# Kernel optimization log

Hardware: AMD Instinct MI355X
Metric: run time of the kernel (lower is better)

## Reference

```python
import jax, jax.numpy as jnp
import numpy as np

B, N, E, H, D, FF, L = 64, 200, 128, 8, 16, 512, 6
S = N + 1  # depot + nodes
EPS = 1e-5


def setup_inputs() -> dict:
    key = jax.random.key(0)
    ks = jax.random.split(key, 24)
    r = jax.random.normal
    HD = H * D
    inp = {
        "depot_xy": jax.random.uniform(ks[0], (B, 1, 3), dtype=jnp.float32),
        "node_xy_demand_tw": jax.random.uniform(ks[1], (B, N, 4), dtype=jnp.float32),
        "route_attn": r(ks[2], (B, H, S, S), dtype=jnp.float32),
        # initial embeddings
        "Wd": r(ks[3], (3, E)) * 0.3, "bd": jnp.zeros((E,)),
        "Wn": r(ks[4], (4, E)) * 0.3, "bn": jnp.zeros((E,)),
        # per-layer stacked params (leading dim L)
        "Wq": r(ks[5], (L, E, HD)) / np.sqrt(E),
        "Wk": r(ks[6], (L, E, HD)) / np.sqrt(E),
        "Wv": r(ks[7], (L, E, HD)) / np.sqrt(E),
        "Wo": r(ks[8], (L, HD, E)) / np.sqrt(HD), "bo": jnp.zeros((L, E)),
        # score_aggr MLP: in=head_num*aspect_num=2H, hidden=2H, out=H
        "A1w": r(ks[9], (L, 2 * H, 2 * H)) / np.sqrt(2 * H), "A1b": jnp.zeros((L, 2 * H)),
        "A2w": r(ks[10], (L, 2 * H, H)) / np.sqrt(2 * H), "A2b": jnp.zeros((L, H)),
        # instance-norm affine params
        "n1w": jnp.ones((L, E)), "n1b": jnp.zeros((L, E)),
        "n2w": jnp.ones((L, E)), "n2b": jnp.zeros((L, E)),
        # feed-forward
        "F1w": r(ks[11], (L, E, FF)) / np.sqrt(E), "F1b": jnp.zeros((L, FF)),
        "F2w": r(ks[12], (L, FF, E)) / np.sqrt(FF), "F2b": jnp.zeros((L, E)),
    }
    return inp


def _inorm(y, w, b):
    # InstanceNorm1d over the sequence axis (per batch, per channel), biased var, eps=1e-5
    m = jnp.mean(y, axis=1, keepdims=True)
    v = jnp.var(y, axis=1, keepdims=True)
    return (y - m) / jnp.sqrt(v + EPS) * w + b


def _encoder(depot_xy, node_xy_demand_tw, route_attn, Wd, bd, Wn, bn,
             Wq, Wk, Wv, Wo, bo, A1w, A1b, A2w, A2b,
             n1w, n1b, n2w, n2b, F1w, F1b, F2w, F2b):
    x = jnp.concatenate([depot_xy @ Wd + bd, node_xy_demand_tw @ Wn + bn], axis=1)  # [B,S,E]
    b, s = x.shape[0], x.shape[1]
    for l in range(L):
        heads = lambda t: t.reshape(b, s, H, D).transpose(0, 2, 1, 3)  # [B,H,S,D]
        q, k, v = heads(x @ Wq[l]), heads(x @ Wk[l]), heads(x @ Wv[l])
        score = jnp.einsum('bhnd,bhmd->bhnm', q, k)                    # [B,H,S,S]
        cat = jnp.concatenate([score, route_attn], axis=1)             # [B,2H,S,S]
        cat = cat.transpose(0, 2, 3, 1)                                # [B,S,S,2H]
        agg = jax.nn.relu(cat @ A1w[l] + A1b[l]) @ A2w[l] + A2b[l]     # [B,S,S,H]
        scaled = agg.transpose(0, 3, 1, 2)                             # [B,H,S,S]
        w = jax.nn.softmax(scaled, axis=-1)
        o = jnp.einsum('bhnm,bhmd->bhnd', w, v)                        # [B,H,S,D]
        o = o.transpose(0, 2, 1, 3).reshape(b, s, H * D)
        mh = o @ Wo[l] + bo[l]
        out1 = _inorm(x + mh, n1w[l], n1b[l])
        ff = jax.nn.relu(out1 @ F1w[l] + F1b[l]) @ F2w[l] + F2b[l]
        x = _inorm(out1 + ff, n2w[l], n2b[l])
    return x


def reference(depot_xy, node_xy_demand_tw, route_attn, Wd, bd, Wn, bn,
              Wq, Wk, Wv, Wo, bo, A1w, A1b, A2w, A2b,
              n1w, n1b, n2w, n2b, F1w, F1b, F2w, F2b):
    return _encoder(depot_xy, node_xy_demand_tw, route_attn, Wd, bd, Wn, bn,
                    Wq, Wk, Wv, Wo, bo, A1w, A1b, A2w, A2b,
                    n1w, n1b, n2w, n2b, F1w, F1b, F2w, F2b)
```

## Files before the change

kernel.cpp:

```cpp
#include <hip/hip_runtime.h>
#include <hip/hip_bf16.h>

#define B_   64
#define N_   200
#define S_   201
#define E_   128
#define H_   8
#define D_   16
#define HD_  128
#define FF_  512
#define L_   6
#define TWOH_ 16
#define NCH_  4
#define NCHB_ 51
#define PADM_ 209
#define QKVW_ 384

typedef __hip_bfloat16 bf16;
typedef __attribute__((ext_vector_type(8))) short bfrag;
typedef __attribute__((ext_vector_type(4))) float f32x4;

__device__ __forceinline__ void split_bf16(float v, bf16& h, bf16& l) {
  h = __float2bfloat16(v);
  l = __float2bfloat16(v - __bfloat162float(h));
}

__device__ __forceinline__ void stage16(const bf16* g, bf16* l) {
  __builtin_amdgcn_global_load_lds(
      (const __attribute__((address_space(1))) void*)g,
      (__attribute__((address_space(3))) void*)l, 16, 0, 0);
}

__global__ void embed_kernel(const float* __restrict__ depot, const float* __restrict__ node,
                             const float* __restrict__ Wd, const float* __restrict__ bd,
                             const float* __restrict__ Wn, const float* __restrict__ bn,
                             float* __restrict__ X, bf16* __restrict__ XBh, bf16* __restrict__ XBl) {
  int idx = blockIdx.x * blockDim.x + threadIdx.x;
  if (idx >= B_ * S_ * E_) return;
  int e  = idx & (E_ - 1);
  int bs = idx >> 7;
  int s  = bs % S_;
  int b  = bs / S_;
  float acc;
  if (s == 0) {
    acc = bd[e];
    #pragma unroll
    for (int i = 0; i < 3; ++i) acc += depot[b * 3 + i] * Wd[i * E_ + e];
  } else {
    acc = bn[e];
    const float* nd = node + ((size_t)b * N_ + (s - 1)) * 4;
    #pragma unroll
    for (int i = 0; i < 4; ++i) acc += nd[i] * Wn[i * E_ + e];
  }
  X[idx] = acc;
  bf16 hh, ll;
  split_bf16(acc, hh, ll);
  XBh[idx] = hh;
  XBl[idx] = ll;
}

__global__ void wcvt_kernel(const float* __restrict__ Wo, const float* __restrict__ F1w,
                            const float* __restrict__ F2w, const float* __restrict__ Wq,
                            const float* __restrict__ Wk, const float* __restrict__ Wv,
                            bf16* __restrict__ WTh, bf16* __restrict__ WTl) {
  int idx = blockIdx.x * blockDim.x + threadIdx.x;
  if (idx >= 1179648) return;
  float v;
  if (idx < 98304) {
    int l = idx / 16384, rr = idx % 16384;
    int e = rr / 128, h = rr % 128;
    v = Wo[(size_t)l * 16384 + h * 128 + e];
  } else if (idx < 491520) {
    int rem = idx - 98304;
    int l = rem / 65536, rr = rem % 65536;
    int f = rr / 128, e = rr % 128;
    v = F1w[(size_t)l * 65536 + e * 512 + f];
  } else if (idx < 884736) {
    int rem = idx - 491520;
    int l = rem / 65536, rr = rem % 65536;
    int e = rr / 512, f = rr % 512;
    v = F2w[(size_t)l * 65536 + f * 128 + e];
  } else {
    int rem = idx - 884736;
    int l = rem / 49152, rr = rem % 49152;
    int n = rr / 128, e = rr % 128;
    const float* src = (n < 128) ? Wq : (n < 256) ? Wk : Wv;
    int hd = n & 127;
    v = src[(size_t)l * 16384 + e * 128 + hd];
  }
  bf16 h, l2;
  split_bf16(v, h, l2);
  WTh[idx] = h;
  WTl[idx] = l2;
}

template<int EPI>
__global__ __launch_bounds__(256) void mgemm_kernel(
    const bf16* __restrict__ Ah, const bf16* __restrict__ Al,
    const bf16* __restrict__ BTh, const bf16* __restrict__ BTl,
    const float* __restrict__ bias, const float* __restrict__ res,
    float* __restrict__ Cf, bf16* __restrict__ Cbh, bf16* __restrict__ Cbl,
    int K, int Ntot, int lda) {
  __shared__ __align__(16) bf16 Ash[4096];
  __shared__ __align__(16) bf16 Asl[4096];
  __shared__ __align__(16) bf16 Bsh[4096];
  __shared__ __align__(16) bf16 Bsl[4096];
  int tid = threadIdx.x;
  int m0 = blockIdx.x * 64, n0 = blockIdx.y * 64;
  int lane = tid & 63, wave = tid >> 6;
  int wr = wave >> 1, wc = wave & 1;
  int la = lane & 15, lb = lane >> 4;
  int lrow = lane >> 3;
  int cbl  = (lane & 7) ^ (lrow & 7);
  f32x4 acc[2][2] = {};
  for (int k0 = 0; k0 < K; k0 += 64) {
    #pragma unroll
    for (int c = 0; c < 2; ++c) {
      int rr = wave * 16 + c * 8 + lrow;
      size_t ga = (size_t)(m0 + rr) * lda + k0 + cbl * 8;
      size_t gb = (size_t)(n0 + rr) * K + k0 + cbl * 8;
      int lo = wave * 1024 + c * 512;
      stage16(Ah + ga, Ash + lo);
      stage16(Al + ga, Asl + lo);
      stage16(BTh + gb, Bsh + lo);
      stage16(BTl + gb, Bsl + lo);
    }
    __syncthreads();
    #pragma unroll
    for (int ks = 0; ks < 64; ks += 32) {
      int cb0 = (ks >> 3) + lb;
      auto rd = [&](const bf16* buf, int r) {
        return *reinterpret_cast<const bfrag*>(&buf[r * 64 + ((cb0 ^ (r & 7)) << 3)]);
      };
      int ra0 = wr * 32 + la, ra1 = ra0 + 16;
      int rb0 = wc * 32 + la, rb1 = rb0 + 16;
      bfrag ah0 = rd(Ash, ra0), ah1 = rd(Ash, ra1);
      bfrag al0 = rd(Asl, ra0), al1 = rd(Asl, ra1);
      bfrag bh0 = rd(Bsh, rb0), bh1 = rd(Bsh, rb1);
      bfrag bl0 = rd(Bsl, rb0), bl1 = rd(Bsl, rb1);
      acc[0][0] = __builtin_amdgcn_mfma_f32_16x16x32_bf16(ah0, bh0, acc[0][0], 0, 0, 0);
      acc[0][0] = __builtin_amdgcn_mfma_f32_16x16x32_bf16(ah0, bl0, acc[0][0], 0, 0, 0);
      acc[0][0] = __builtin_amdgcn_mfma_f32_16x16x32_bf16(al0, bh0, acc[0][0], 0, 0, 0);
      acc[0][1] = __builtin_amdgcn_mfma_f32_16x16x32_bf16(ah0, bh1, acc[0][1], 0, 0, 0);
      acc[0][1] = __builtin_amdgcn_mfma_f32_16x16x32_bf16(ah0, bl1, acc[0][1], 0, 0, 0);
      acc[0][1] = __builtin_amdgcn_mfma_f32_16x16x32_bf16(al0, bh1, acc[0][1], 0, 0, 0);
      acc[1][0] = __builtin_amdgcn_mfma_f32_16x16x32_bf16(ah1, bh0, acc[1][0], 0, 0, 0);
      acc[1][0] = __builtin_amdgcn_mfma_f32_16x16x32_bf16(ah1, bl0, acc[1][0], 0, 0, 0);
      acc[1][0] = __builtin_amdgcn_mfma_f32_16x16x32_bf16(al1, bh0, acc[1][0], 0, 0, 0);
      acc[1][1] = __builtin_amdgcn_mfma_f32_16x16x32_bf16(ah1, bh1, acc[1][1], 0, 0, 0);
      acc[1][1] = __builtin_amdgcn_mfma_f32_16x16x32_bf16(ah1, bl1, acc[1][1], 0, 0, 0);
      acc[1][1] = __builtin_amdgcn_mfma_f32_16x16x32_bf16(al1, bh1, acc[1][1], 0, 0, 0);
    }
    __syncthreads();
  }
  int r0 = lb * 4;
  #pragma unroll
  for (int ti = 0; ti < 2; ++ti)
    #pragma unroll
    for (int tj = 0; tj < 2; ++tj)
      #pragma unroll
      for (int j = 0; j < 4; ++j) {
        int m = m0 + wr * 32 + ti * 16 + r0 + j;
        int n = n0 + wc * 32 + tj * 16 + la;
        float v = acc[ti][tj][j];
        if (EPI == 1) {
          v += bias[n] + res[(size_t)m * Ntot + n];
          Cf[(size_t)m * Ntot + n] = v;
        } else if (EPI == 2) {
          v += bias[n];
          v = v > 0.f ? v : 0.f;
          bf16 vh, vl;
          split_bf16(v, vh, vl);
          Cbh[(size_t)m * Ntot + n] = vh;
          Cbl[(size_t)m * Ntot + n] = vl;
        } else {
          Cf[(size_t)m * Ntot + n] = v;
        }
      }
}

__global__ __launch_bounds__(256) void score_kernel(const float* __restrict__ QKV,
                                                    float* __restrict__ SC) {
  int bh = blockIdx.x;
  int h = bh & 7, b = bh >> 3;
  int nbase = blockIdx.y * 51;
  int ncnt = min(51, S_ - nbase);
  __shared__ __align__(16) float qs[51][20];
  __shared__ __align__(16) float ks[S_][20];
  int tid = threadIdx.x;
  for (int p = tid; p < 51 * 16; p += 256) {
    int r = p >> 4, d = p & 15;
    if (r < ncnt) qs[r][d] = QKV[((size_t)(b * S_ + nbase + r)) * QKVW_ + h * D_ + d];
  }
  for (int p = tid; p < S_ * 16; p += 256) {
    int r = p >> 4, d = p & 15;
    ks[r][d] = QKV[((size_t)(b * S_ + r)) * QKVW_ + 128 + h * D_ + d];
  }
  __syncthreads();
  float* out = SC + ((size_t)(b * H_ + h)) * S_ * S_;
  int tn = tid >> 4, tm = tid & 15;
  for (int n0 = tn * 2; n0 < ncnt; n0 += 32) {
    int n1v = (n0 + 1 < ncnt);
    f32x4 q0[4], q1[4];
    #pragma unroll
    for (int qd = 0; qd < 4; ++qd) {
      q0[qd] = *(const f32x4*)&qs[n0][qd * 4];
      q1[qd] = *(const f32x4*)&qs[n1v ? n0 + 1 : n0][qd * 4];
    }
    for (int m0 = tm * 2; m0 < S_; m0 += 32) {
      int m1v = (m0 + 1 < S_);
      float a00 = 0, a01 = 0, a10 = 0, a11 = 0;
      #pragma unroll
      for (int qd = 0; qd < 4; ++qd) {
        f32x4 k0 = *(const f32x4*)&ks[m0][qd * 4];
        f32x4 k1 = *(const f32x4*)&ks[m1v ? m0 + 1 : m0][qd * 4];
        #pragma unroll
        for (int c = 0; c < 4; ++c) {
          a00 += q0[qd][c] * k0[c];
          a01 += q0[qd][c] * k1[c];
          a10 += q1[qd][c] * k0[c];
          a11 += q1[qd][c] * k1[c];
        }
      }
      int gn = nbase + n0;
      out[(size_t)gn * S_ + m0] = a00;
      if (m1v) out[(size_t)gn * S_ + m0 + 1] = a01;
      if (n1v) {
        out[(size_t)(gn + 1) * S_ + m0] = a10;
        if (m1v) out[(size_t)(gn + 1) * S_ + m0 + 1] = a11;
      }
    }
  }
}

__global__ __launch_bounds__(256) void attn_kernel(
    const float* __restrict__ SC, const float* __restrict__ RA,
    const float* __restrict__ A1w, const float* __restrict__ A1b,
    const float* __restrict__ A2w, const float* __restrict__ A2b,
    float* __restrict__ QKV) {
  int blk = blockIdx.x;
  int b  = blk / NCHB_;
  int n0 = (blk % NCHB_) * NCH_;
  int NV = min(NCH_, S_ - n0);
  __shared__ float PL[NCH_][H_][PADM_];
  __shared__ float partial[2][NCH_][H_][D_];
  __shared__ float inv[NCH_][H_];
  int tid = threadIdx.x;

  {
    float cc[4][TWOH_];
    int   mm[4], nnv[4];
    bool  val[4];
    #pragma unroll
    for (int s = 0; s < 4; ++s) {
      int e = tid + s * 256;
      val[s] = (e < NV * S_);
      int nn = e / S_;
      int m  = e - nn * S_;
      if (!val[s]) { nn = 0; m = 0; }
      nnv[s] = nn; mm[s] = m;
      const float* scp = SC + (((size_t)b * H_) * S_ + (n0 + nn)) * S_ + m;
      const float* rap = RA + (((size_t)b * H_) * S_ + (n0 + nn)) * S_ + m;
      #pragma unroll
      for (int h = 0; h < H_; ++h) {
        cc[s][h]      = scp[(size_t)h * S_ * S_];
        cc[s][H_ + h] = rap[(size_t)h * S_ * S_];
      }
    }
    #pragma unroll
    for (int s = 0; s < 4; ++s) {
      if (!val[s]) continue;
      float h1[TWOH_];
      #pragma unroll
      for (int j = 0; j < TWOH_; ++j) h1[j] = A1b[j];
      #pragma unroll
      for (int i = 0; i < TWOH_; ++i) {
        float c = cc[s][i];
        #pragma unroll
        for (int j = 0; j < TWOH_; ++j)
          h1[j] += c * A1w[i * TWOH_ + j];
      }
      float agg[H_];
      #pragma unroll
      for (int h = 0; h < H_; ++h) agg[h] = A2b[h];
      #pragma unroll
      for (int j = 0; j < TWOH_; ++j) {
        float r = fmaxf(h1[j], 0.f);
        #pragma unroll
        for (int h = 0; h < H_; ++h)
          agg[h] += r * A2w[j * H_ + h];
      }
      #pragma unroll
      for (int h = 0; h < H_; ++h) PL[nnv[s]][h][mm[s]] = agg[h];
    }
  }
  __syncthreads();

  {
    int g = tid >> 3, lane = tid & 7;
    int nn = g >> 3, h = g & 7;
    if (nn < NV) {
      float mx = -1e30f;
      for (int m = lane; m < S_; m += 8) mx = fmaxf(mx, PL[nn][h][m]);
      #pragma unroll
      for (int off = 4; off > 0; off >>= 1) mx = fmaxf(mx, __shfl_xor(mx, off, 8));
      float sum = 0.f;
      for (int m = lane; m < S_; m += 8) {
        float e = __expf(PL[nn][h][m] - mx);
        PL[nn][h][m] = e;
        sum += e;
      }
      #pragma unroll
      for (int off = 4; off > 0; off >>= 1) sum += __shfl_xor(sum, off, 8);
      if (lane == 0) inv[nn][h] = 1.f / sum;
    }
  }
  __syncthreads();

  {
    int half = tid >> 7, h = (tid >> 4) & 7, d = tid & 15;
    float a0 = 0.f, a1 = 0.f, a2 = 0.f, a3 = 0.f;
    const float* vp = QKV + (size_t)b * S_ * QKVW_ + 256 + h * D_ + d;
    for (int m = half; m < S_; m += 2) {
      float vv = vp[(size_t)m * QKVW_];
      a0 += PL[0][h][m] * vv;
      a1 += PL[1][h][m] * vv;
      a2 += PL[2][h][m] * vv;
      a3 += PL[3][h][m] * vv;
    }
    partial[half][0][h][d] = a0;
    partial[half][1][h][d] = a1;
    partial[half][2][h][d] = a2;
    partial[half][3][h][d] = a3;
  }
  __syncthreads();
  if (tid < 128) {
    int h = tid >> 4, d = tid & 15;
    #pragma unroll
    for (int nn = 0; nn < NCH_; ++nn)
      if (nn < NV) {
        float s = (partial[0][nn][h][d] + partial[1][nn][h][d]) * inv[nn][h];
        bf16* ob = (bf16*)(QKV + (size_t)(b * S_ + n0 + nn) * QKVW_);
        bf16 sh, sl;
        split_bf16(s, sh, sl);
        ob[h * D_ + d]       = sh;
        ob[128 + h * D_ + d] = sl;
      }
  }
}

__global__ __launch_bounds__(128) void inorm_kernel(const float* __restrict__ Y,
                                                    const float* __restrict__ w,
                                                    const float* __restrict__ bb,
                                                    float* __restrict__ X,
                                                    bf16* __restrict__ XBh,
                                                    bf16* __restrict__ XBl) {
  int b = blockIdx.x;
  int e0 = blockIdx.y * 32;
  int tid = threadIdx.x;
  int el = tid & 31, sg = tid >> 5;
  int e = e0 + el;
  __shared__ float ps[4][32], pss[4][32];
  const float* base = Y + (size_t)b * S_ * E_;
  float s = 0.f, ss = 0.f;
  for (int i = sg; i < S_; i += 4) {
    float v = base[(size_t)i * E_ + e];
    s += v; ss += v * v;
  }
  ps[sg][el] = s; pss[sg][el] = ss;
  __syncthreads();
  if (sg == 0) {
    s  = ps[0][el] + ps[1][el] + ps[2][el] + ps[3][el];
    ss = pss[0][el] + pss[1][el] + pss[2][el] + pss[3][el];
    float mean = s / S_;
    float var  = fmaxf(ss / S_ - mean * mean, 0.f);
    float scale = rsqrtf(var + 1e-5f) * w[e];
    ps[0][el]  = scale;
    pss[0][el] = bb[e] - mean * scale;
  }
  __syncthreads();
  float scale = ps[0][el], shift = pss[0][el];
  float* dst = X + (size_t)b * S_ * E_;
  for (int i = sg; i < S_; i += 4) {
    size_t idx = (size_t)i * E_ + e;
    float v = base[idx] * scale + shift;
    dst[idx] = v;
    if (XBh) {
      size_t gi = (size_t)b * S_ * E_ + idx;
      bf16 vh, vl;
      split_bf16(v, vh, vl);
      XBh[gi] = vh;
      XBl[gi] = vl;
    }
  }
}

extern "C" void kernel_launch(void* const* d_in, const int* in_sizes, int n_in,
                              void* d_out, int out_size, void* d_ws, size_t ws_size,
                              hipStream_t stream) {
  const float* depot = (const float*)d_in[0];
  const float* node  = (const float*)d_in[1];
  const float* RA    = (const float*)d_in[2];
  const float* Wd    = (const float*)d_in[3];
  const float* bd    = (const float*)d_in[4];
  const float* Wn    = (const float*)d_in[5];
  const float* bn    = (const float*)d_in[6];
  const float* Wq    = (const float*)d_in[7];
  const float* Wk    = (const float*)d_in[8];
  const float* Wv    = (const float*)d_in[9];
  const float* Wo    = (const float*)d_in[10];
  const float* bo    = (const float*)d_in[11];
  const float* A1w   = (const float*)d_in[12];
  const float* A1b   = (const float*)d_in[13];
  const float* A2w   = (const float*)d_in[14];
  const float* A2b   = (const float*)d_in[15];
  const float* n1w   = (const float*)d_in[16];
  const float* n1b   = (const float*)d_in[17];
  const float* n2w   = (const float*)d_in[18];
  const float* n2b   = (const float*)d_in[19];
  const float* F1w   = (const float*)d_in[20];
  const float* F1b   = (const float*)d_in[21];
  const float* F2w   = (const float*)d_in[22];
  const float* F2b   = (const float*)d_in[23];

  const size_t XSZ  = (size_t)B_ * S_ * E_;
  const size_t SCSZ = (size_t)B_ * H_ * S_ * S_;
  const size_t XBF  = XSZ / 2;
  float* ws = (float*)d_ws;
  float* X   = ws;
  float* QKV = ws + XSZ;
  float* SC  = ws + 4 * XSZ;
  float* TMP = SC;
  bf16*  XBh = (bf16*)(SC + XSZ);
  bf16*  XBl = (bf16*)(SC + XSZ + XBF);
  bf16*  HBh = (bf16*)(SC + XSZ + 2 * XBF);
  bf16*  HBl = (bf16*)(SC + XSZ + 6 * XBF);
  float* tail = ws + 4 * XSZ + SCSZ;
  bf16*  WTh = (bf16*)tail;
  bf16*  WTl = (bf16*)(tail + 589824);
  const bf16* OBh = (const bf16*)QKV;
  const bf16* OBl = (const bf16*)QKV + 128;

  const int M = B_ * S_;

  wcvt_kernel<<<4608, 256, 0, stream>>>(Wo, F1w, F2w, Wq, Wk, Wv, WTh, WTl);
  embed_kernel<<<(B_ * S_ * E_ + 255) / 256, 256, 0, stream>>>(depot, node, Wd, bd, Wn, bn, X, XBh, XBl);

  for (int l = 0; l < L_; ++l) {
    mgemm_kernel<3><<<dim3(M / 64, 6), 256, 0, stream>>>(
        XBh, XBl, WTh + 884736 + (size_t)l * 49152, WTl + 884736 + (size_t)l * 49152,
        nullptr, nullptr, QKV, nullptr, nullptr, E_, QKVW_, E_);
    score_kernel<<<dim3(B_ * H_, 4), 256, 0, stream>>>(QKV, SC);
    attn_kernel<<<B_ * NCHB_, 256, 0, stream>>>(SC, RA,
        A1w + (size_t)l * TWOH_ * TWOH_, A1b + (size_t)l * TWOH_,
        A2w + (size_t)l * TWOH_ * H_,    A2b + (size_t)l * H_, QKV);
    mgemm_kernel<1><<<dim3(M / 64, 2), 256, 0, stream>>>(
        OBh, OBl, WTh + (size_t)l * 16384, WTl + (size_t)l * 16384,
        bo + (size_t)l * E_, X, TMP, nullptr, nullptr, HD_, E_, 768);
    inorm_kernel<<<dim3(B_, 4), 128, 0, stream>>>(TMP, n1w + (size_t)l * E_, n1b + (size_t)l * E_, X, XBh, XBl);
    mgemm_kernel<2><<<dim3(M / 64, 8), 256, 0, stream>>>(
        XBh, XBl, WTh + 98304 + (size_t)l * 65536, WTl + 98304 + (size_t)l * 65536,
        F1b + (size_t)l * FF_, nullptr, nullptr, HBh, HBl, E_, FF_, E_);
    mgemm_kernel<1><<<dim3(M / 64, 2), 256, 0, stream>>>(
        HBh, HBl, WTh + 491520 + (size_t)l * 65536, WTl + 491520 + (size_t)l * 65536,
        F2b + (size_t)l * E_, X, TMP, nullptr, nullptr, FF_, E_, FF_);
    float* dst = (l == L_ - 1) ? (float*)d_out : X;
    bf16* xh = (l == L_ - 1) ? nullptr : XBh;
    bf16* xl = (l == L_ - 1) ? nullptr : XBl;
    inorm_kernel<<<dim3(B_, 4), 128, 0, stream>>>(TMP, n2w + (size_t)l * E_, n2b + (size_t)l * E_, dst, xh, xl);
  }
}
```

Measured before the change: 1.476 ms.

## Fuse QK score computation into attention kernel, dropping score buffer

Result: faster. 1.358 ms (-8.0%).

```diff
diff --git a/kernel.cpp b/kernel.cpp
--- a/kernel.cpp
+++ b/kernel.cpp
@@ -179,62 +179,8 @@
       }
 }
 
-__global__ __launch_bounds__(256) void score_kernel(const float* __restrict__ QKV,
-                                                    float* __restrict__ SC) {
-  int bh = blockIdx.x;
-  int h = bh & 7, b = bh >> 3;
-  int nbase = blockIdx.y * 51;
-  int ncnt = min(51, S_ - nbase);
-  __shared__ __align__(16) float qs[51][20];
-  __shared__ __align__(16) float ks[S_][20];
-  int tid = threadIdx.x;
-  for (int p = tid; p < 51 * 16; p += 256) {
-    int r = p >> 4, d = p & 15;
-    if (r < ncnt) qs[r][d] = QKV[((size_t)(b * S_ + nbase + r)) * QKVW_ + h * D_ + d];
-  }
-  for (int p = tid; p < S_ * 16; p += 256) {
-    int r = p >> 4, d = p & 15;
-    ks[r][d] = QKV[((size_t)(b * S_ + r)) * QKVW_ + 128 + h * D_ + d];
-  }
-  __syncthreads();
-  float* out = SC + ((size_t)(b * H_ + h)) * S_ * S_;
-  int tn = tid >> 4, tm = tid & 15;
-  for (int n0 = tn * 2; n0 < ncnt; n0 += 32) {
-    int n1v = (n0 + 1 < ncnt);
-    f32x4 q0[4], q1[4];
-    #pragma unroll
-    for (int qd = 0; qd < 4; ++qd) {
-      q0[qd] = *(const f32x4*)&qs[n0][qd * 4];
-      q1[qd] = *(const f32x4*)&qs[n1v ? n0 + 1 : n0][qd * 4];
-    }
-    for (int m0 = tm * 2; m0 < S_; m0 += 32) {
-      int m1v = (m0 + 1 < S_);
-      float a00 = 0, a01 = 0, a10 = 0, a11 = 0;
-      #pragma unroll
-      for (int qd = 0; qd < 4; ++qd) {
-        f32x4 k0 = *(const f32x4*)&ks[m0][qd * 4];
-        f32x4 k1 = *(const f32x4*)&ks[m1v ? m0 + 1 : m0][qd * 4];
-        #pragma unroll
-        for (int c = 0; c < 4; ++c) {
-          a00 += q0[qd][c] * k0[c];
-          a01 += q0[qd][c] * k1[c];
-          a10 += q1[qd][c] * k0[c];
-          a11 += q1[qd][c] * k1[c];
-        }
-      }
-      int gn = nbase + n0;
-      out[(size_t)gn * S_ + m0] = a00;
-      if (m1v) out[(size_t)gn * S_ + m0 + 1] = a01;
-      if (n1v) {
-        out[(size_t)(gn + 1) * S_ + m0] = a10;
-        if (m1v) out[(size_t)(gn + 1) * S_ + m0 + 1] = a11;
-      }
-    }
-  }
-}
-
 __global__ __launch_bounds__(256) void attn_kernel(
-    const float* __restrict__ SC, const float* __restrict__ RA,
+    const float* __restrict__ RA,
     const float* __restrict__ A1w, const float* __restrict__ A1b,
     const float* __restrict__ A2w, const float* __restrict__ A2b,
     float* __restrict__ QKV) {
@@ -243,9 +189,40 @@
   int n0 = (blk % NCHB_) * NCH_;
   int NV = min(NCH_, S_ - n0);
   __shared__ float PL[NCH_][H_][PADM_];
-  __shared__ float partial[2][NCH_][H_][D_];
-  __shared__ float inv[NCH_][H_];
+  __shared__ float shbuf[1056];
+  float* qs  = shbuf;
+  float* inv = shbuf + 1024;
   int tid = threadIdx.x;
+
+  for (int p = tid; p < NV * HD_; p += 256) {
+    int nn = p >> 7, d = p & 127;
+    qs[nn * HD_ + d] = QKV[((size_t)(b * S_ + n0 + nn)) * QKVW_ + d];
+  }
+  __syncthreads();
+
+  for (int p = tid; p < H_ * S_; p += 256) {
+    int h = p / S_, m = p - h * S_;
+    const float* kp = QKV + ((size_t)(b * S_ + m)) * QKVW_ + 128 + h * D_;
+    f32x4 k0 = *(const f32x4*)(kp + 0);
+    f32x4 k1 = *(const f32x4*)(kp + 4);
+    f32x4 k2 = *(const f32x4*)(kp + 8);
+    f32x4 k3 = *(const f32x4*)(kp + 12);
+    #pragma unroll
+    for (int nn = 0; nn < NCH_; ++nn) {
+      const float* q = qs + nn * HD_ + h * D_;
+      float a = 0.f;
+      #pragma unroll
+      for (int c = 0; c < 4; ++c) a += q[c] * k0[c];
+      #pragma unroll
+      for (int c = 0; c < 4; ++c) a += q[4 + c] * k1[c];
+      #pragma unroll
+      for (int c = 0; c < 4; ++c) a += q[8 + c] * k2[c];
+      #pragma unroll
+      for (int c = 0; c < 4; ++c) a += q[12 + c] * k3[c];
+      PL[nn][h][m] = a;
+    }
+  }
+  __syncthreads();
 
   {
     float cc[4][TWOH_];
@@ -259,11 +236,10 @@
       int m  = e - nn * S_;
       if (!val[s]) { nn = 0; m = 0; }
       nnv[s] = nn; mm[s] = m;
-      const float* scp = SC + (((size_t)b * H_) * S_ + (n0 + nn)) * S_ + m;
       const float* rap = RA + (((size_t)b * H_) * S_ + (n0 + nn)) * S_ + m;
       #pragma unroll
       for (int h = 0; h < H_; ++h) {
-        cc[s][h]      = scp[(size_t)h * S_ * S_];
+        cc[s][h]      = PL[nn][h][m];
         cc[s][H_ + h] = rap[(size_t)h * S_ * S_];
       }
     }
@@ -312,11 +288,12 @@
       }
       #pragma unroll
       for (int off = 4; off > 0; off >>= 1) sum += __shfl_xor(sum, off, 8);
-      if (lane == 0) inv[nn][h] = 1.f / sum;
-    }
-  }
-  __syncthreads();
-
+      if (lane == 0) inv[nn * H_ + h] = 1.f / sum;
+    }
+  }
+  __syncthreads();
+
+  float (*partial)[NCH_][H_][D_] = (float (*)[NCH_][H_][D_])shbuf;
   {
     int half = tid >> 7, h = (tid >> 4) & 7, d = tid & 15;
     float a0 = 0.f, a1 = 0.f, a2 = 0.f, a3 = 0.f;
@@ -339,7 +316,7 @@
     #pragma unroll
     for (int nn = 0; nn < NCH_; ++nn)
       if (nn < NV) {
-        float s = (partial[0][nn][h][d] + partial[1][nn][h][d]) * inv[nn][h];
+        float s = (partial[0][nn][h][d] + partial[1][nn][h][d]) * inv[nn * H_ + h];
         bf16* ob = (bf16*)(QKV + (size_t)(b * S_ + n0 + nn) * QKVW_);
         bf16 sh, sl;
         split_bf16(s, sh, sl);
@@ -429,12 +406,12 @@
   float* ws = (float*)d_ws;
   float* X   = ws;
   float* QKV = ws + XSZ;
-  float* SC  = ws + 4 * XSZ;
-  float* TMP = SC;
-  bf16*  XBh = (bf16*)(SC + XSZ);
-  bf16*  XBl = (bf16*)(SC + XSZ + XBF);
-  bf16*  HBh = (bf16*)(SC + XSZ + 2 * XBF);
-  bf16*  HBl = (bf16*)(SC + XSZ + 6 * XBF);
+  float* SCR = ws + 4 * XSZ;
+  float* TMP = SCR;
+  bf16*  XBh = (bf16*)(SCR + XSZ);
+  bf16*  XBl = (bf16*)(SCR + XSZ + XBF);
+  bf16*  HBh = (bf16*)(SCR + XSZ + 2 * XBF);
+  bf16*  HBl = (bf16*)(SCR + XSZ + 6 * XBF);
   float* tail = ws + 4 * XSZ + SCSZ;
   bf16*  WTh = (bf16*)tail;
   bf16*  WTl = (bf16*)(tail + 589824);
@@ -450,8 +427,7 @@
     mgemm_kernel<3><<<dim3(M / 64, 6), 256, 0, stream>>>(
         XBh, XBl, WTh + 884736 + (size_t)l * 49152, WTl + 884736 + (size_t)l * 49152,
         nullptr, nullptr, QKV, nullptr, nullptr, E_, QKVW_, E_);
-    score_kernel<<<dim3(B_ * H_, 4), 256, 0, stream>>>(QKV, SC);
-    attn_kernel<<<B_ * NCHB_, 256, 0, stream>>>(SC, RA,
+    attn_kernel<<<B_ * NCHB_, 256, 0, stream>>>(RA,
         A1w + (size_t)l * TWOH_ * TWOH_, A1b + (size_t)l * TWOH_,
         A2w + (size_t)l * TWOH_ * H_,    A2b + (size_t)l * H_, QKV);
     mgemm_kernel<1><<<dim3(M / 64, 2), 256, 0, stream>>>(
```
